# Performance work log

Hardware: AMD Instinct MI355X
Metric: run time of the kernel (lower is better)

## Reference

```python
import jax, jax.numpy as jnp
import numpy as np

N = 10000      # nodes
E = 160000     # edges (before self-loops)
F_IN = 128     # num_features
H1, D1 = 4, 256   # conv1: 4 heads x 256, concat -> 1024
D2 = 256          # conv2: 1 head x 256
NEG_SLOPE = 0.2


def setup_inputs() -> dict:
    key = jax.random.key(0)
    ks = jax.random.split(key, 12)
    def p(k, shape, fan):
        return jax.random.normal(k, shape, jnp.float32) / np.float32(np.sqrt(fan))
    return {
        "x": jax.random.normal(ks[0], (N, F_IN), jnp.float32),
        "edge_index": jax.random.randint(ks[1], (2, E), 0, N, jnp.int32),
        "W1": p(ks[2], (F_IN, H1 * D1), F_IN),
        "att_src1": p(ks[3], (H1, D1), D1),
        "att_dst1": p(ks[4], (H1, D1), D1),
        "b1": jnp.zeros((H1 * D1,), jnp.float32),
        "lin1_W": p(ks[5], (F_IN, H1 * D1), F_IN),
        "lin1_b": jnp.zeros((H1 * D1,), jnp.float32),
        "W2": p(ks[6], (H1 * D1, D2), H1 * D1),
        "att_src2": p(ks[7], (1, D2), D2),
        "att_dst2": p(ks[8], (1, D2), D2),
        "b2": jnp.zeros((D2,), jnp.float32),
        "lin2_W": p(ks[9], (H1 * D1, D2), H1 * D1),
        "lin2_b": jnp.zeros((D2,), jnp.float32),
    }


def gat_layer(x, src, dst, W, a_src, a_dst, b, heads, d):
    """PyG-style GATConv: transform, edgewise LeakyReLU attention,
    segment-softmax over destination neighborhoods, scatter-add, concat heads."""
    n = x.shape[0]
    h = (x @ W).reshape(n, heads, d)                       # [N, H, D]
    s_src = jnp.einsum('nhd,hd->nh', h, a_src)             # per-node scores
    s_dst = jnp.einsum('nhd,hd->nh', h, a_dst)
    e = jax.nn.leaky_relu(s_src[src] + s_dst[dst], NEG_SLOPE)   # [E, H]
    m = jax.ops.segment_max(e, dst, num_segments=n)        # stable softmax per dst
    p = jnp.exp(e - m[dst])
    z = jax.ops.segment_sum(p, dst, num_segments=n)
    alpha = p / (z[dst] + 1e-16)                           # [E, H]
    msg = h[src] * alpha[:, :, None]                       # [E, H, D]
    out = jax.ops.segment_sum(msg, dst, num_segments=n)    # [N, H, D]
    return out.reshape(n, heads * d) + b, alpha


def reference(x, edge_index, W1, att_src1, att_dst1, b1, lin1_W, lin1_b,
              W2, att_src2, att_dst2, b2, lin2_W, lin2_b):
    n = x.shape[0]
    loop = jnp.arange(n, dtype=edge_index.dtype)           # add self-loops (PyG default)
    src = jnp.concatenate([edge_index[0], loop])
    dst = jnp.concatenate([edge_index[1], loop])
    h1, alpha1 = gat_layer(x, src, dst, W1, att_src1, att_dst1, b1, H1, D1)
    h1 = jax.nn.elu(h1 + x @ lin1_W + lin1_b)              # conv1 + lin1 residual, ELU
    h2, _ = gat_layer(h1, src, dst, W2, att_src2, att_dst2, b2, 1, D2)
    out = h2 + h1 @ lin2_W + lin2_b                        # conv2 + lin2 residual
    return out, alpha1
```

## Files before the change

kernel.cpp:

```cpp
#include <hip/hip_runtime.h>
#include <hip/hip_bf16.h>
#include <math.h>

#define NN   10000
#define EE   160000
#define ETOT 170000
#define FIN  128
#define C1   1024
#define NH1  4
#define D1   256
#define D2   256
#define MAXD 96

typedef __attribute__((ext_vector_type(8))) short bf16x8;
typedef __attribute__((ext_vector_type(4))) float f32x4;

__device__ __forceinline__ float b2f(unsigned short u)
{
    union { unsigned int i; float f; } c; c.i = (unsigned int)u << 16; return c.f;
}
__device__ __forceinline__ unsigned short f2b(float x)
{
    return __builtin_bit_cast(unsigned short, __float2bfloat16(x));
}
__device__ __forceinline__ void split1(float x, unsigned short &h, unsigned short &l)
{
    __hip_bfloat16 hb = __float2bfloat16(x);
    float r = x - __bfloat162float(hb);
    h = __builtin_bit_cast(unsigned short, hb);
    l = __builtin_bit_cast(unsigned short, __float2bfloat16(r));
}

__device__ __forceinline__ void split_A_body(const float* __restrict__ X,
                                             unsigned short* __restrict__ A2,
                                             int M, int K, int idx)
{
    int kq4 = K >> 2;
    if (idx >= M * kq4) return;
    int m = idx / kq4, kq = idx % kq4;
    float4 v = *(const float4*)&X[(size_t)m * K + kq * 4];
    ushort4 h, l;
    split1(v.x, h.x, l.x); split1(v.y, h.y, l.y);
    split1(v.z, h.z, l.z); split1(v.w, h.w, l.w);
    unsigned short* row = A2 + (size_t)m * (2 * K);
    *(ushort4*)&row[kq * 4]     = h;
    *(ushort4*)&row[K + kq * 4] = l;
}

__device__ __forceinline__ void split_Bt_body(const float* __restrict__ B0,
                                              const float* __restrict__ B1,
                                              int K, int N0, int Ntot,
                                              unsigned short* __restrict__ Bt, int idx)
{
    int total = Ntot * (K >> 2);
    if (idx >= total) return;
    int n = idx % Ntot;
    int kq = idx / Ntot;
    int k = kq * 4;
    const float* B; int nc, nb;
    if (n < N0) { B = B0; nc = n; nb = N0; }
    else        { B = B1; nc = n - N0; nb = Ntot - N0; }
    float v0 = B[(size_t)(k + 0) * nb + nc];
    float v1 = B[(size_t)(k + 1) * nb + nc];
    float v2 = B[(size_t)(k + 2) * nb + nc];
    float v3 = B[(size_t)(k + 3) * nb + nc];
    ushort4 h, l;
    split1(v0, h.x, l.x); split1(v1, h.y, l.y);
    split1(v2, h.z, l.z); split1(v3, h.w, l.w);
    unsigned short* row = Bt + (size_t)n * (3 * K);
    *(ushort4*)&row[k]         = h;
    *(ushort4*)&row[K + k]     = h;
    *(ushort4*)&row[2 * K + k] = l;
}

__device__ __forceinline__ void split_Bt1_body(const float* __restrict__ W1,
                                               const float* __restrict__ lin1W,
                                               unsigned short* __restrict__ Bt, int idx)
{
    if (idx >= 1024 * 64) return;
    int n = idx & 1023;
    int k = (idx >> 10) * 4;
    float v[4];
    #pragma unroll
    for (int i = 0; i < 4; ++i) {
        int kk = k + i;
        v[i] = (kk < 128) ? W1[(size_t)kk * C1 + n] : lin1W[(size_t)(kk - 128) * C1 + n];
    }
    ushort4 h, l;
    split1(v[0], h.x, l.x); split1(v[1], h.y, l.y);
    split1(v[2], h.z, l.z); split1(v[3], h.w, l.w);
    unsigned short* row = Bt + (size_t)n * 768;
    *(ushort4*)&row[k]       = h;
    *(ushort4*)&row[256 + k] = h;
    *(ushort4*)&row[512 + k] = l;
}

__global__ __launch_bounds__(256)
void prep(const float* __restrict__ x, unsigned short* __restrict__ A1stk,
          const float* __restrict__ W1, const float* __restrict__ lin1_W,
          unsigned short* __restrict__ Bt1,
          const float* __restrict__ W2, const float* __restrict__ lin2_W,
          unsigned short* __restrict__ Bt2,
          const int* __restrict__ dstp, int* __restrict__ cnt,
          const float* __restrict__ as1, const float* __restrict__ ad1,
          float* __restrict__ w1s, float* __restrict__ w1d,
          const float* __restrict__ as2, const float* __restrict__ ad2,
          float* __restrict__ v2s, float* __restrict__ v2d)
{
    const int b = blockIdx.x, t = threadIdx.x;
    const int w = t >> 6, lane = t & 63;
    if (b < 1250) {
        split_A_body(x, A1stk, NN, FIN, b * 256 + t);
    } else if (b < 1506) {
        split_Bt1_body(W1, lin1_W, Bt1, (b - 1250) * 256 + t);
    } else if (b < 2018) {
        split_Bt_body(W2, lin2_W, C1, D2, 512, Bt2, (b - 1506) * 256 + t);
    } else if (b < 2683) {
        int e = (b - 2018) * 256 + t;
        if (e < ETOT) {
            int d = (e < EE) ? dstp[e] : (e - EE);
            atomicAdd(&cnt[d], 1);
        }
    } else if (b < 2939) {
        int gw = (b - 2683) * 4 + w;
        int k = gw >> 3, rem = gw & 7, h = rem >> 1, issd = rem & 1;
        const float* a = issd ? ad1 : as1;
        float4 wv = *(const float4*)&W1[(size_t)k * C1 + h * 256 + lane * 4];
        float4 av = *(const float4*)&a[h * 256 + lane * 4];
        float s = wv.x * av.x + wv.y * av.y + wv.z * av.z + wv.w * av.w;
        #pragma unroll
        for (int off = 32; off; off >>= 1) s += __shfl_xor(s, off);
        if (lane == 0) (issd ? w1d : w1s)[k * 4 + h] = s;
    } else {
        int gw = (b - 2939) * 4 + w;
        int k = gw >> 1, issd = gw & 1;
        const float* a = issd ? ad2 : as2;
        float4 wv = *(const float4*)&W2[(size_t)k * D2 + lane * 4];
        float4 av = *(const float4*)&a[lane * 4];
        float s = wv.x * av.x + wv.y * av.y + wv.z * av.z + wv.w * av.w;
        #pragma unroll
        for (int off = 32; off; off >>= 1) s += __shfl_xor(s, off);
        if (lane == 0) (issd ? v2d : v2s)[k] = s;
    }
}

__device__ __forceinline__ void glds16(const void* g, void* l)
{
    __builtin_amdgcn_global_load_lds((const __attribute__((address_space(1))) void*)g,
                                     (__attribute__((address_space(3))) void*)l, 16, 0, 0);
}

__global__ __launch_bounds__(256)
void gemm_l1(const unsigned short* __restrict__ Apx,
             const unsigned short* __restrict__ Ax,
             const unsigned short* __restrict__ Bt,
             unsigned short* __restrict__ h1split,
             int M, const float* __restrict__ bias0, const float* __restrict__ bias1)
{
    constexpr int BM = 128, BN = 128, BK = 32;
    constexpr int FJ = 4, FI = 4;
    constexpr int SLOTS = 4, SMASK = 3, SWSH = 1;
    constexpr int RPC = 16, ACH = 8, CPW = 4;
    constexpr int ABUF = BM * BK, BBUF = BN * BK;
    __shared__ __align__(16) unsigned short sA[2 * ABUF];
    __shared__ __align__(16) unsigned short sB[2 * BBUF];
    const int tid = threadIdx.x, w = tid >> 6, lane = tid & 63;
    const int cpx = gridDim.x >> 3;
    const int t0 = (blockIdx.x & 7) * cpx + (blockIdx.x >> 3);
    const int m0 = (t0 >> 3) * BM;
    const int n0 = (t0 & 7) * BN;
    const int hsel = n0 >> 8;
    const int wm = w >> 1, wn = w & 1;
    f32x4 acc[FI][FJ] = {};

    const unsigned short *gx[CPW], *gpx[CPW], *gb[CPW];
    int lofs[CPW]; bool isa[CPW];
    {
        const int r = lane / SLOTS, sl = lane % SLOTS;
        const int ssl = sl ^ ((r >> SWSH) & SMASK);
        #pragma unroll
        for (int cc = 0; cc < CPW; ++cc) {
            int c = w * CPW + cc;
            if (c < ACH) {
                int gm = m0 + c * RPC + r; if (gm >= M) gm = M - 1;
                gx[cc]  = Ax  + (size_t)gm * 256 + ssl * 8;
                gpx[cc] = Apx + (size_t)gm * 1024 + hsel * 256 + ssl * 8;
                gb[cc]  = nullptr;
                lofs[cc] = c * 512;
                isa[cc] = true;
            } else {
                int gn = n0 + (c - ACH) * RPC + r;
                gx[cc] = gpx[cc] = nullptr;
                gb[cc] = Bt + (size_t)gn * 768 + ssl * 8;
                lofs[cc] = (c - ACH) * 512;
                isa[cc] = false;
            }
        }
    }

    const int rAl = wm * 64 + (lane & 15);
    const int rBl = wn * 64 + (lane & 15);
    const int sIdx = lane >> 4;
    const int nit = 768 / BK;
    int cur = 0;

    auto stage = [&](int kk, int buf) {
        int rr = kk >> 7;
        bool px = !(rr & 1);
        int off = px ? ((rr == 2) ? 128 : 0) : ((rr == 3) ? 128 : 0);
        int kin = kk & 127;
        #pragma unroll
        for (int cc = 0; cc < CPW; ++cc) {
            if (isa[cc]) glds16((px ? gpx[cc] : gx[cc]) + off + kin, sA + buf * ABUF + lofs[cc]);
            else         glds16(gb[cc] + kk,                         sB + buf * BBUF + lofs[cc]);
        }
    };

    stage(0, 0);
    __syncthreads();
    for (int it = 0; it < nit; ++it) {
        if (it + 1 < nit) stage((it + 1) * BK, cur ^ 1);
        const unsigned short* cA = sA + cur * ABUF;
        const unsigned short* cB = sB + cur * BBUF;
        bf16x8 av[FJ], bv[FI];
        #pragma unroll
        for (int f = 0; f < FI; ++f) {
            int row = rBl + f * 16;
            bv[f] = *(const bf16x8*)&cB[row * BK + ((sIdx ^ ((row >> SWSH) & SMASK)) << 3)];
        }
        #pragma unroll
        for (int f = 0; f < FJ; ++f) {
            int row = rAl + f * 16;
            av[f] = *(const bf16x8*)&cA[row * BK + ((sIdx ^ ((row >> SWSH) & SMASK)) << 3)];
        }
        #pragma unroll
        for (int fj = 0; fj < FJ; ++fj)
            #pragma unroll
            for (int fi = 0; fi < FI; ++fi)
                acc[fi][fj] = __builtin_amdgcn_mfma_f32_16x16x32_bf16(
                    bv[fi], av[fj], acc[fi][fj], 0, 0, 0);
        __syncthreads();
        cur ^= 1;
    }

    const int lrow = lane & 15;
    const int lcol = (lane >> 4) << 2;
    #pragma unroll
    for (int fj = 0; fj < FJ; ++fj) {
        int row = m0 + wm * 64 + fj * 16 + lrow;
        if (row >= M) continue;
        #pragma unroll
        for (int fi = 0; fi < FI; ++fi) {
            int col = n0 + wn * 64 + fi * 16 + lcol;
            f32x4 v = acc[fi][fj];
            const float4 g0 = *(const float4*)&bias0[col];
            const float4 g1 = *(const float4*)&bias1[col];
            v[0] += g0.x + g1.x; v[1] += g0.y + g1.y;
            v[2] += g0.z + g1.z; v[3] += g0.w + g1.w;
            #pragma unroll
            for (int i = 0; i < 4; ++i) v[i] = v[i] > 0.f ? v[i] : expm1f(v[i]);
            ushort4 hi, lo;
            split1(v[0], hi.x, lo.x); split1(v[1], hi.y, lo.y);
            split1(v[2], hi.z, lo.z); split1(v[3], hi.w, lo.w);
            unsigned short* orow = h1split + (size_t)row * 2048;
            *(ushort4*)&orow[col]        = hi;
            *(ushort4*)&orow[C1 + col]   = lo;
        }
    }
}

template<int BN, int WM, int WN, int BK>
__global__ __launch_bounds__(256)
void gemm_split(const unsigned short* __restrict__ A, int lda, int ka2,
                const unsigned short* __restrict__ Bt, int keff,
                unsigned short* __restrict__ outPb, float* __restrict__ outR,
                int M, int nsplit, int ldR, int ntn,
                const float* __restrict__ bias0, const float* __restrict__ bias1)
{
    constexpr int BM   = 128;
    constexpr int WTM  = BM / WM,  WTN = BN / WN;
    constexpr int FJ   = WTM / 16, FI  = WTN / 16;
    constexpr int KS   = BK / 32;
    constexpr int SLOTS = BK / 8;
    constexpr int SMASK = SLOTS - 1;
    constexpr int SWSH  = (BK == 32) ? 1 : 0;
    constexpr int RPC  = 512 / BK;
    constexpr int ACH  = BM / RPC;
    constexpr int NCH  = (BM + BN) / RPC;
    constexpr int CPW  = NCH / 4;
    constexpr int ABUF = BM * BK, BBUF = BN * BK;

    __shared__ __align__(16) unsigned short sA[2 * ABUF];
    __shared__ __align__(16) unsigned short sB[2 * BBUF];

    const int tid = threadIdx.x;
    const int w = tid >> 6, lane = tid & 63;

    const int cpx = gridDim.x >> 3;
    const int t0  = (blockIdx.x & 7) * cpx + (blockIdx.x >> 3);
    const int m0 = (t0 / ntn) * BM;
    const int n0 = (t0 % ntn) * BN;
    const int wm = w / WN, wn = w % WN;

    f32x4 acc[FI][FJ] = {};

    const unsigned short* gp[CPW];
    int lofs[CPW];
    bool isa[CPW];
    {
        const int r  = lane / SLOTS;
        const int sl = lane % SLOTS;
        const int ssl = sl ^ ((r >> SWSH) & SMASK);
        #pragma unroll
        for (int cc = 0; cc < CPW; ++cc) {
            int c = w * CPW + cc;
            if (c < ACH) {
                int gm = m0 + c * RPC + r; if (gm >= M) gm = M - 1;
                gp[cc]   = A + (size_t)gm * lda + ssl * 8;
                lofs[cc] = c * 512;
                isa[cc]  = true;
            } else {
                int gn = n0 + (c - ACH) * RPC + r;
                gp[cc]   = Bt + (size_t)gn * keff + ssl * 8;
                lofs[cc] = (c - ACH) * 512;
                isa[cc]  = false;
            }
        }
    }

    const int rAl = wm * WTM + (lane & 15);
    const int rBl = wn * WTN + (lane & 15);
    const int koff = (lane >> 4) * 8;
    const int nit = keff / BK;
    int cur = 0;

    #pragma unroll
    for (int cc = 0; cc < CPW; ++cc)
        glds16(gp[cc], (isa[cc] ? sA : sB) + lofs[cc]);
    __syncthreads();

    for (int it = 0; it < nit; ++it) {
        if (it + 1 < nit) {
            int kn = (it + 1) * BK;
            int kAn = (kn >= ka2) ? (kn - ka2) : kn;
            #pragma unroll
            for (int cc = 0; cc < CPW; ++cc) {
                unsigned short* dst = (isa[cc] ? sA + (cur ^ 1) * ABUF
                                               : sB + (cur ^ 1) * BBUF) + lofs[cc];
                glds16(gp[cc] + (isa[cc] ? kAn : kn), dst);
            }
        }
        const unsigned short* cA = sA + cur * ABUF;
        const unsigned short* cB = sB + cur * BBUF;
        #pragma unroll
        for (int ks = 0; ks < KS; ++ks) {
            const int sIdx = (ks * 32 + koff) >> 3;
            bf16x8 av[FJ], bv[FI];
            #pragma unroll
            for (int f = 0; f < FI; ++f) {
                int row = rBl + f * 16;
                bv[f] = *(const bf16x8*)&cB[row * BK + ((sIdx ^ ((row >> SWSH) & SMASK)) << 3)];
            }
            #pragma unroll
            for (int f = 0; f < FJ; ++f) {
                int row = rAl + f * 16;
                av[f] = *(const bf16x8*)&cA[row * BK + ((sIdx ^ ((row >> SWSH) & SMASK)) << 3)];
            }
            #pragma unroll
            for (int fj = 0; fj < FJ; ++fj)
                #pragma unroll
                for (int fi = 0; fi < FI; ++fi)
                    acc[fi][fj] = __builtin_amdgcn_mfma_f32_16x16x32_bf16(
                        bv[fi], av[fj], acc[fi][fj], 0, 0, 0);
        }
        __syncthreads();
        cur ^= 1;
    }

    const int lrow = lane & 15;
    const int lcol = (lane >> 4) << 2;
    #pragma unroll
    for (int fj = 0; fj < FJ; ++fj) {
        int row = m0 + wm * WTM + fj * 16 + lrow;
        if (row >= M) continue;
        #pragma unroll
        for (int fi = 0; fi < FI; ++fi) {
            int col = n0 + wn * WTN + fi * 16 + lcol;
            f32x4 v = acc[fi][fj];
            if (col < nsplit) {
                ushort4 o;
                o.x = f2b(v[0]); o.y = f2b(v[1]); o.z = f2b(v[2]); o.w = f2b(v[3]);
                *(ushort4*)&outPb[(size_t)row * nsplit + col] = o;
            } else {
                int c = col - nsplit;
                const float4 g0 = *(const float4*)&bias0[c];
                const float4 g1 = *(const float4*)&bias1[c];
                v[0] += g0.x + g1.x; v[1] += g0.y + g1.y;
                v[2] += g0.z + g1.z; v[3] += g0.w + g1.w;
                *(f32x4*)&outR[(size_t)row * ldR + c] = v;
            }
        }
    }
}

__global__ __launch_bounds__(256)
void s1_scores(const float* __restrict__ x, const float* __restrict__ w1s,
               const float* __restrict__ w1d, float* __restrict__ s_src,
               float* __restrict__ s_dst)
{
    const int n = blockIdx.x * 4 + (threadIdx.x >> 6);
    if (n >= NN) return;
    const int lane = threadIdx.x & 63;
    float2 xv = *(const float2*)&x[(size_t)n * FIN + lane * 2];
    float4 wa = *(const float4*)&w1s[(lane * 2) * 4];
    float4 wb = *(const float4*)&w1s[(lane * 2 + 1) * 4];
    float4 da = *(const float4*)&w1d[(lane * 2) * 4];
    float4 db = *(const float4*)&w1d[(lane * 2 + 1) * 4];
    float ss[4] = { xv.x * wa.x + xv.y * wb.x, xv.x * wa.y + xv.y * wb.y,
                    xv.x * wa.z + xv.y * wb.z, xv.x * wa.w + xv.y * wb.w };
    float sd[4] = { xv.x * da.x + xv.y * db.x, xv.x * da.y + xv.y * db.y,
                    xv.x * da.z + xv.y * db.z, xv.x * da.w + xv.y * db.w };
    #pragma unroll
    for (int off = 32; off; off >>= 1) {
        #pragma unroll
        for (int h = 0; h < 4; ++h) {
            ss[h] += __shfl_xor(ss[h], off);
            sd[h] += __shfl_xor(sd[h], off);
        }
    }
    if (lane == 0) {
        #pragma unroll
        for (int h = 0; h < 4; ++h) {
            s_src[n * NH1 + h] = ss[h];
            s_dst[n * NH1 + h] = sd[h];
        }
    }
}

__global__ __launch_bounds__(256)
void scores2(const unsigned short* __restrict__ h1split, const float* __restrict__ v2s,
             const float* __restrict__ v2d, float* __restrict__ s_src,
             float* __restrict__ s_dst)
{
    const int n = blockIdx.x * 4 + (threadIdx.x >> 6);
    if (n >= NN) return;
    const int lane = threadIdx.x & 63;
    const unsigned short* row = h1split + (size_t)n * 2048 + lane * 16;
    float ss = 0.f, sd = 0.f;
    #pragma unroll
    for (int q = 0; q < 16; ++q) {
        float hv = b2f(row[q]);
        ss += hv * v2s[lane * 16 + q];
        sd += hv * v2d[lane * 16 + q];
    }
    #pragma unroll
    for (int off = 32; off; off >>= 1) {
        ss += __shfl_xor(ss, off);
        sd += __shfl_xor(sd, off);
    }
    if (lane == 0) { s_src[n] = ss; s_dst[n] = sd; }
}

__global__ __launch_bounds__(1024)
void scan_kernel(const int* __restrict__ cnt, int* __restrict__ row_ptr)
{
    __shared__ int part[1024];
    const int t = threadIdx.x;
    int local[10];
    int s = 0;
    #pragma unroll
    for (int j = 0; j < 10; ++j) {
        int idx = t * 10 + j;
        local[j] = s;
        s += (idx < NN) ? cnt[idx] : 0;
    }
    part[t] = s;
    __syncthreads();
    for (int off = 1; off < 1024; off <<= 1) {
        int v = (t >= off) ? part[t - off] : 0;
        __syncthreads();
        part[t] += v;
        __syncthreads();
    }
    int prefix = (t > 0) ? part[t - 1] : 0;
    #pragma unroll
    for (int j = 0; j < 10; ++j) {
        int idx = t * 10 + j;
        if (idx < NN) row_ptr[idx] = prefix + local[j];
    }
    if (t == 0) row_ptr[NN] = ETOT;
}

__global__ void scatter_edges(const int* __restrict__ srcp, const int* __restrict__ dstp,
                              const int* __restrict__ row_ptr, int* __restrict__ fill,
                              int* __restrict__ csr_src, int* __restrict__ csr_eid)
{
    int e = blockIdx.x * 256 + threadIdx.x;
    if (e >= ETOT) return;
    int s, d;
    if (e < EE) { s = srcp[e]; d = dstp[e]; } else { s = d = e - EE; }
    int pos = row_ptr[d] + atomicAdd(&fill[d], 1);
    csr_src[pos] = s;
    csr_eid[pos] = e;
}

__global__ __launch_bounds__(256)
void px_gather(const unsigned short* __restrict__ Ax, const float* __restrict__ s_src,
               const float* __restrict__ s_dst, const int* __restrict__ row_ptr,
               const int* __restrict__ csr_src, const int* __restrict__ csr_eid,
               unsigned short* __restrict__ Apx, float* __restrict__ alpha_out)
{
    __shared__ float lalpha[NH1][MAXD];
    const int n = blockIdx.x;
    const int t = threadIdx.x;
    const int h = t >> 6;
    const int lane = t & 63;
    const int start = row_ptr[n], end = row_ptr[n + 1];
    const float sd = s_dst[n * NH1 + h];

    float m = -1e30f;
    for (int i = start + lane; i < end; i += 64) {
        float sc = s_src[csr_src[i] * NH1 + h] + sd;
        sc = sc > 0.f ? sc : 0.2f * sc;
        m = fmaxf(m, sc);
    }
    #pragma unroll
    for (int off = 32; off; off >>= 1) m = fmaxf(m, __shfl_xor(m, off));
    float z = 0.f;
    for (int i = start + lane; i < end; i += 64) {
        float sc = s_src[csr_src[i] * NH1 + h] + sd;
        sc = sc > 0.f ? sc : 0.2f * sc;
        z += __expf(sc - m);
    }
    #pragma unroll
    for (int off = 32; off; off >>= 1) z += __shfl_xor(z, off);
    const float invz = 1.f / (z + 1e-16f);
    for (int i = start + lane; i < end; i += 64) {
        float sc = s_src[csr_src[i] * NH1 + h] + sd;
        sc = sc > 0.f ? sc : 0.2f * sc;
        float a = __expf(sc - m) * invz;
        alpha_out[(size_t)csr_eid[i] * NH1 + h] = a;
        int idx = i - start;
        if (idx < MAXD) lalpha[h][idx] = a;
    }
    __syncthreads();

    float p0 = 0.f, p1 = 0.f;
    for (int i = start; i < end; ++i) {
        const int s = csr_src[i];
        const int idx = i - start;
        float a;
        if (idx < MAXD) {
            a = lalpha[h][idx];
        } else {
            float sc = s_src[s * NH1 + h] + sd;
            sc = sc > 0.f ? sc : 0.2f * sc;
            a = __expf(sc - m) * invz;
        }
        const unsigned short* xr = Ax + (size_t)s * 256 + lane * 2;
        ushort2 xh = *(const ushort2*)xr;
        ushort2 xl = *(const ushort2*)(xr + 128);
        p0 += a * (b2f(xh.x) + b2f(xl.x));
        p1 += a * (b2f(xh.y) + b2f(xl.y));
    }
    ushort2 hi, lo;
    split1(p0, hi.x, lo.x);
    split1(p1, hi.y, lo.y);
    unsigned short* orow = Apx + (size_t)n * 1024 + h * 256 + lane * 2;
    *(ushort2*)orow         = hi;
    *(ushort2*)(orow + 128) = lo;
}

__global__ __launch_bounds__(64)
void aggregate2(const unsigned short* __restrict__ h2b, const float* __restrict__ s_src,
                const float* __restrict__ s_dst,
                const int* __restrict__ row_ptr, const int* __restrict__ csr_src,
                const float* __restrict__ accin, float* __restrict__ out)
{
    __shared__ float lalpha[MAXD];
    const int n = blockIdx.x;
    const int t = threadIdx.x;
    const int start = row_ptr[n], end = row_ptr[n + 1];
    const float sd = s_dst[n];

    float m = -1e30f;
    for (int i = start + t; i < end; i += 64) {
        float sc = s_src[csr_src[i]] + sd;
        sc = sc > 0.f ? sc : 0.2f * sc;
        m = fmaxf(m, sc);
    }
    #pragma unroll
    for (int off = 32; off; off >>= 1) m = fmaxf(m, __shfl_xor(m, off));
    float z = 0.f;
    for (int i = start + t; i < end; i += 64) {
        float sc = s_src[csr_src[i]] + sd;
        sc = sc > 0.f ? sc : 0.2f * sc;
        z += __expf(sc - m);
    }
    #pragma unroll
    for (int off = 32; off; off >>= 1) z += __shfl_xor(z, off);
    const float invz = 1.f / (z + 1e-16f);
    for (int i = start + t; i < end; i += 64) {
        float sc = s_src[csr_src[i]] + sd;
        sc = sc > 0.f ? sc : 0.2f * sc;
        int idx = i - start;
        if (idx < MAXD) lalpha[idx] = __expf(sc - m) * invz;
    }
    __syncthreads();

    float4 acc = make_float4(0.f, 0.f, 0.f, 0.f);
    for (int i = start; i < end; ++i) {
        const int s = csr_src[i];
        const int idx = i - start;
        float a;
        if (idx < MAXD) {
            a = lalpha[idx];
        } else {
            float sc = s_src[s] + sd;
            sc = sc > 0.f ? sc : 0.2f * sc;
            a = __expf(sc - m) * invz;
        }
        ushort4 v = *(const ushort4*)&h2b[(size_t)s * D2 + t * 4];
        acc.x += a * b2f(v.x); acc.y += a * b2f(v.y);
        acc.z += a * b2f(v.z); acc.w += a * b2f(v.w);
    }
    float4 base = *(const float4*)&accin[(size_t)n * D2 + t * 4];
    float4 r;
    r.x = acc.x + base.x; r.y = acc.y + base.y;
    r.z = acc.z + base.z; r.w = acc.w + base.w;
    *(float4*)&out[(size_t)n * D2 + t * 4] = r;
}

extern "C" void kernel_launch(void* const* d_in, const int* in_sizes, int n_in,
                              void* d_out, int out_size, void* d_ws, size_t ws_size,
                              hipStream_t stream)
{
    const float* x        = (const float*)d_in[0];
    const int*   ei       = (const int*)  d_in[1];
    const float* W1       = (const float*)d_in[2];
    const float* att_src1 = (const float*)d_in[3];
    const float* att_dst1 = (const float*)d_in[4];
    const float* b1       = (const float*)d_in[5];
    const float* lin1_W   = (const float*)d_in[6];
    const float* lin1_b   = (const float*)d_in[7];
    const float* W2       = (const float*)d_in[8];
    const float* att_src2 = (const float*)d_in[9];
    const float* att_dst2 = (const float*)d_in[10];
    const float* b2       = (const float*)d_in[11];
    const float* lin2_W   = (const float*)d_in[12];
    const float* lin2_b   = (const float*)d_in[13];
    const int* srcp = ei;
    const int* dstp = ei + EE;

    float* out    = (float*)d_out;
    float* alpha1 = out + (size_t)NN * D2;

    float* fw = (float*)d_ws;
    unsigned short* A1stk = (unsigned short*)fw; fw += (size_t)NN * 256 / 2;
    unsigned short* Apx   = (unsigned short*)fw; fw += (size_t)NN * 1024 / 2;
    unsigned short* A2stk = (unsigned short*)fw; fw += (size_t)NN * 2048 / 2;
    unsigned short* h2b   = (unsigned short*)fw; fw += (size_t)NN * 256 / 2;
    float* acc2   = fw;  fw += (size_t)NN * D2;
    unsigned short* Bt1 = (unsigned short*)fw; fw += (size_t)1024 * 768 / 2;
    unsigned short* Bt2 = (unsigned short*)fw; fw += (size_t)512 * 3072 / 2;
    float* w1s = fw; fw += 512;
    float* w1d = fw; fw += 512;
    float* v2s = fw; fw += 1024;
    float* v2d = fw; fw += 1024;
    float* s_src1 = fw; fw += NN * NH1;
    float* s_dst1 = fw; fw += NN * NH1;
    float* s_src2 = fw; fw += NN;
    float* s_dst2 = fw; fw += NN;
    int* ip      = (int*)fw;
    int* cnt     = ip;  ip += NN;
    int* fill    = ip;  ip += NN;
    int* row_ptr = ip;  ip += NN + 4;
    int* csr_src = ip;  ip += ETOT;
    int* csr_eid = ip;  ip += ETOT;

    hipMemsetAsync(cnt, 0, 2 * NN * sizeof(int), stream);

    prep<<<3451, 256, 0, stream>>>(x, A1stk, W1, lin1_W, Bt1, W2, lin2_W, Bt2,
                                   dstp, cnt, att_src1, att_dst1, w1s, w1d,
                                   att_src2, att_dst2, v2s, v2d);

    scan_kernel<<<1, 1024, 0, stream>>>(cnt, row_ptr);
    scatter_edges<<<(ETOT + 255) / 256, 256, 0, stream>>>(srcp, dstp, row_ptr, fill,
                                                          csr_src, csr_eid);

    s1_scores<<<(NN + 3) / 4, 256, 0, stream>>>(x, w1s, w1d, s_src1, s_dst1);
    px_gather<<<NN, 256, 0, stream>>>(A1stk, s_src1, s_dst1, row_ptr, csr_src, csr_eid,
                                      Apx, alpha1);

    gemm_l1<<<79 * 8, 256, 0, stream>>>(Apx, A1stk, Bt1, A2stk, NN, lin1_b, b1);

    scores2<<<(NN + 3) / 4, 256, 0, stream>>>(A2stk, v2s, v2d, s_src2, s_dst2);

    gemm_split<64, 4, 1, 64><<<79 * 8, 256, 0, stream>>>(
        A2stk, 2 * C1, 2 * C1, Bt2, 3 * C1, h2b, acc2, NN, D2, D2, 8, lin2_b, b2);

    aggregate2<<<NN, 64, 0, stream>>>(h2b, s_src2, s_dst2, row_ptr, csr_src, acc2, out);
}
```

Baseline: 223.0 us.

## Parallelize neighbor gathers across edges and read fp32 x directly

Both gather kernels are restructured so different lanes process different edges in parallel, and results are combined with shuffle and shared-memory reductions. Previously each wave walked the edges one at a time. px_gather now reads fp32 x rows (8 floats per lane) and reuses each row load for all four heads, instead of loading a bf16 hi/lo split row separately per head. aggregate2 uses 4 edge slots with 16-wide bf16 vector loads. The aim is more memory-level parallelism and less per-edge latency, at the cost of more registers and extra reduction work.

```diff
diff --git a/kernel.cpp b/kernel.cpp
--- a/kernel.cpp
+++ b/kernel.cpp
@@ -505,70 +505,116 @@
 }
 
 __global__ __launch_bounds__(256)
-void px_gather(const unsigned short* __restrict__ Ax, const float* __restrict__ s_src,
+void px_gather(const float* __restrict__ x, const float* __restrict__ s_src,
                const float* __restrict__ s_dst, const int* __restrict__ row_ptr,
                const int* __restrict__ csr_src, const int* __restrict__ csr_eid,
                unsigned short* __restrict__ Apx, float* __restrict__ alpha_out)
 {
     __shared__ float lalpha[NH1][MAXD];
+    __shared__ float lmz[NH1][2];
+    __shared__ float red[4][16][33];
     const int n = blockIdx.x;
     const int t = threadIdx.x;
-    const int h = t >> 6;
+    const int w = t >> 6;
     const int lane = t & 63;
     const int start = row_ptr[n], end = row_ptr[n + 1];
-    const float sd = s_dst[n * NH1 + h];
-
-    float m = -1e30f;
-    for (int i = start + lane; i < end; i += 64) {
-        float sc = s_src[csr_src[i] * NH1 + h] + sd;
-        sc = sc > 0.f ? sc : 0.2f * sc;
-        m = fmaxf(m, sc);
-    }
-    #pragma unroll
-    for (int off = 32; off; off >>= 1) m = fmaxf(m, __shfl_xor(m, off));
-    float z = 0.f;
-    for (int i = start + lane; i < end; i += 64) {
-        float sc = s_src[csr_src[i] * NH1 + h] + sd;
-        sc = sc > 0.f ? sc : 0.2f * sc;
-        z += __expf(sc - m);
-    }
-    #pragma unroll
-    for (int off = 32; off; off >>= 1) z += __shfl_xor(z, off);
-    const float invz = 1.f / (z + 1e-16f);
-    for (int i = start + lane; i < end; i += 64) {
-        float sc = s_src[csr_src[i] * NH1 + h] + sd;
-        sc = sc > 0.f ? sc : 0.2f * sc;
-        float a = __expf(sc - m) * invz;
-        alpha_out[(size_t)csr_eid[i] * NH1 + h] = a;
-        int idx = i - start;
-        if (idx < MAXD) lalpha[h][idx] = a;
+
+    {
+        const int h = w;
+        const float sd = s_dst[n * NH1 + h];
+        float m = -1e30f;
+        for (int i = start + lane; i < end; i += 64) {
+            float sc = s_src[csr_src[i] * NH1 + h] + sd;
+            sc = sc > 0.f ? sc : 0.2f * sc;
+            m = fmaxf(m, sc);
+        }
+        #pragma unroll
+        for (int off = 32; off; off >>= 1) m = fmaxf(m, __shfl_xor(m, off));
+        float z = 0.f;
+        for (int i = start + lane; i < end; i += 64) {
+            float sc = s_src[csr_src[i] * NH1 + h] + sd;
+            sc = sc > 0.f ? sc : 0.2f * sc;
+            z += __expf(sc - m);
+        }
+        #pragma unroll
+        for (int off = 32; off; off >>= 1) z += __shfl_xor(z, off);
+        const float invz = 1.f / (z + 1e-16f);
+        for (int i = start + lane; i < end; i += 64) {
+            float sc = s_src[csr_src[i] * NH1 + h] + sd;
+            sc = sc > 0.f ? sc : 0.2f * sc;
+            float a = __expf(sc - m) * invz;
+            alpha_out[(size_t)csr_eid[i] * NH1 + h] = a;
+            int idx = i - start;
+            if (idx < MAXD) lalpha[h][idx] = a;
+        }
+        if (lane == 0) { lmz[h][0] = m; lmz[h][1] = invz; }
     }
     __syncthreads();
 
-    float p0 = 0.f, p1 = 0.f;
-    for (int i = start; i < end; ++i) {
+    const int slot = w * 4 + (lane >> 4);
+    const int g = lane & 15;
+    float a0, a1, a2, a3;
+    float acc[4][8] = {};
+    for (int i = start + slot; i < end; i += 16) {
         const int s = csr_src[i];
         const int idx = i - start;
-        float a;
         if (idx < MAXD) {
-            a = lalpha[h][idx];
+            a0 = lalpha[0][idx]; a1 = lalpha[1][idx];
+            a2 = lalpha[2][idx]; a3 = lalpha[3][idx];
         } else {
-            float sc = s_src[s * NH1 + h] + sd;
-            sc = sc > 0.f ? sc : 0.2f * sc;
-            a = __expf(sc - m) * invz;
-        }
-        const unsigned short* xr = Ax + (size_t)s * 256 + lane * 2;
-        ushort2 xh = *(const ushort2*)xr;
-        ushort2 xl = *(const ushort2*)(xr + 128);
-        p0 += a * (b2f(xh.x) + b2f(xl.x));
-        p1 += a * (b2f(xh.y) + b2f(xl.y));
-    }
-    ushort2 hi, lo;
-    split1(p0, hi.x, lo.x);
-    split1(p1, hi.y, lo.y);
-    unsigned short* orow = Apx + (size_t)n * 1024 + h * 256 + lane * 2;
-    *(ushort2*)orow         = hi;
-    *(ushort2*)(orow + 128) = lo;
+            #pragma unroll
+            for (int h = 0; h < 4; ++h) {
+                float sc = s_src[s * NH1 + h] + s_dst[n * NH1 + h];
+                sc = sc > 0.f ? sc : 0.2f * sc;
+                float a = __expf(sc - lmz[h][0]) * lmz[h][1];
+                if (h == 0) a0 = a; else if (h == 1) a1 = a;
+                else if (h == 2) a2 = a; else a3 = a;
+            }
+        }
+        const float* xr = &x[(size_t)s * FIN + g * 8];
+        float4 v0 = *(const float4*)&xr[0];
+        float4 v1 = *(const float4*)&xr[4];
+        float vv[8] = { v0.x, v0.y, v0.z, v0.w, v1.x, v1.y, v1.z, v1.w };
+        #pragma unroll
+        for (int d = 0; d < 8; ++d) {
+            acc[0][d] += a0 * vv[d];
+            acc[1][d] += a1 * vv[d];
+            acc[2][d] += a2 * vv[d];
+            acc[3][d] += a3 * vv[d];
+        }
+    }
+    #pragma unroll
+    for (int off = 16; off <= 32; off <<= 1)
+        #pragma unroll
+        for (int h = 0; h < 4; ++h)
+            #pragma unroll
+            for (int d = 0; d < 8; ++d)
+                acc[h][d] += __shfl_xor(acc[h][d], off);
+    if ((lane >> 4) == 0) {
+        #pragma unroll
+        for (int h = 0; h < 4; ++h)
+            #pragma unroll
+            for (int d = 0; d < 8; ++d)
+                red[w][g][h * 8 + d] = acc[h][d];
+    }
+    __syncthreads();
+    if (lane < 16) {
+        float sum[8];
+        #pragma unroll
+        for (int d = 0; d < 8; ++d)
+            sum[d] = red[0][lane][w * 8 + d] + red[1][lane][w * 8 + d]
+                   + red[2][lane][w * 8 + d] + red[3][lane][w * 8 + d];
+        ushort4 hi0, hi1, lo0, lo1;
+        split1(sum[0], hi0.x, lo0.x); split1(sum[1], hi0.y, lo0.y);
+        split1(sum[2], hi0.z, lo0.z); split1(sum[3], hi0.w, lo0.w);
+        split1(sum[4], hi1.x, lo1.x); split1(sum[5], hi1.y, lo1.y);
+        split1(sum[6], hi1.z, lo1.z); split1(sum[7], hi1.w, lo1.w);
+        unsigned short* orow = Apx + (size_t)n * 1024 + w * 256 + lane * 8;
+        *(ushort4*)&orow[0]       = hi0;
+        *(ushort4*)&orow[4]       = hi1;
+        *(ushort4*)&orow[128]     = lo0;
+        *(ushort4*)&orow[132]     = lo1;
+    }
 }
 
 __global__ __launch_bounds__(64)
@@ -608,8 +654,9 @@
     }
     __syncthreads();
 
-    float4 acc = make_float4(0.f, 0.f, 0.f, 0.f);
-    for (int i = start; i < end; ++i) {
+    const int slot = t >> 4, g = t & 15;
+    float acc[16] = {};
+    for (int i = start + slot; i < end; i += 4) {
         const int s = csr_src[i];
         const int idx = i - start;
         float a;
@@ -620,15 +667,32 @@
             sc = sc > 0.f ? sc : 0.2f * sc;
             a = __expf(sc - m) * invz;
         }
-        ushort4 v = *(const ushort4*)&h2b[(size_t)s * D2 + t * 4];
-        acc.x += a * b2f(v.x); acc.y += a * b2f(v.y);
-        acc.z += a * b2f(v.z); acc.w += a * b2f(v.w);
-    }
-    float4 base = *(const float4*)&accin[(size_t)n * D2 + t * 4];
-    float4 r;
-    r.x = acc.x + base.x; r.y = acc.y + base.y;
-    r.z = acc.z + base.z; r.w = acc.w + base.w;
-    *(float4*)&out[(size_t)n * D2 + t * 4] = r;
+        const unsigned short* vr = &h2b[(size_t)s * D2 + g * 16];
+        bf16x8 u0 = *(const bf16x8*)&vr[0];
+        bf16x8 u1 = *(const bf16x8*)&vr[8];
+        #pragma unroll
+        for (int d = 0; d < 8; ++d) {
+            acc[d]     += a * b2f((unsigned short)u0[d]);
+            acc[8 + d] += a * b2f((unsigned short)u1[d]);
+        }
+    }
+    #pragma unroll
+    for (int off = 16; off <= 32; off <<= 1)
+        #pragma unroll
+        for (int d = 0; d < 16; ++d)
+            acc[d] += __shfl_xor(acc[d], off);
+    if (slot == 0) {
+        const float* br = &accin[(size_t)n * D2 + g * 16];
+        float* orow = &out[(size_t)n * D2 + g * 16];
+        #pragma unroll
+        for (int q = 0; q < 4; ++q) {
+            float4 b = *(const float4*)&br[q * 4];
+            float4 r;
+            r.x = acc[q * 4 + 0] + b.x; r.y = acc[q * 4 + 1] + b.y;
+            r.z = acc[q * 4 + 2] + b.z; r.w = acc[q * 4 + 3] + b.w;
+            *(float4*)&orow[q * 4] = r;
+        }
+    }
 }
 
 extern "C" void kernel_launch(void* const* d_in, const int* in_sizes, int n_in,
@@ -689,7 +753,7 @@
                                                           csr_src, csr_eid);
 
     s1_scores<<<(NN + 3) / 4, 256, 0, stream>>>(x, w1s, w1d, s_src1, s_dst1);
-    px_gather<<<NN, 256, 0, stream>>>(A1stk, s_src1, s_dst1, row_ptr, csr_src, csr_eid,
+    px_gather<<<NN, 256, 0, stream>>>(x, s_src1, s_dst1, row_ptr, csr_src, csr_eid,
                                       Apx, alpha1);
 
     gemm_l1<<<79 * 8, 256, 0, stream>>>(Apx, A1stk, Bt1, A2stk, NN, lin1_b, b1);
```

Result: no change. 218.9 us (-1.8%).
